# Kernel optimization log

Measured on AMD Instinct MI355X. Metric: run time of the kernel, lower is better.

The kernel has to match this reference:

```python
import jax, jax.numpy as jnp
from jax import lax
import numpy as np

SEQ_LEN = 96; PRED_LEN = 96; SIGNAL_LEN = 16; NUM_NODES = 256
EMBED = 128; HIDDEN = 64; K_NN = 8; S_SCALE = 2.0; CHEB_ORDER = 2
MA_K = 3; BATCH = 16
C_FREQ = SIGNAL_LEN // 2 + 1          # 9 rfft bins
M_NODES = NUM_NODES * C_FREQ          # nodes per sample graph


def _sin_posemb(pos, dim):
    half = dim // 2
    freqs = 1.0 / (10000.0 ** (np.arange(half) / half))
    ang = pos[:, None] * freqs[None, :]
    return np.concatenate([np.sin(ang), np.cos(ang)], axis=-1).astype(np.float32)


def setup_inputs():
    key = jax.random.key(0)
    ks = jax.random.split(key, 12)
    x = jax.random.normal(ks[0], (BATCH, SEQ_LEN, NUM_NODES), jnp.float32)
    # Chebyshev (order 2) approx of Haar framelet filters cos(xi/2), sin(xi/2) on [0, pi]
    t = np.linspace(-1.0, 1.0, 201); xi = (t + 1.0) * np.pi / 2.0
    ch = np.polynomial.chebyshev
    approx = np.stack([ch.chebfit(t, np.cos(xi / 2.0), CHEB_ORDER),
                       ch.chebfit(t, np.sin(xi / 2.0), CHEB_ORDER)]).astype(np.float32)
    freq_emb = _sin_posemb(np.arange(C_FREQ, dtype=np.float32) * S_SCALE, EMBED)
    sc = (2.0 / EMBED) ** 0.5
    return dict(
        x=x,
        approx=jnp.asarray(approx),                 # [F=2, K=3]
        theta=jnp.ones((2,), jnp.float32),
        fr_Wr=jax.random.normal(ks[1], (EMBED, EMBED), jnp.float32) * sc,
        fr_Wi=jax.random.normal(ks[2], (EMBED, EMBED), jnp.float32) * sc,
        eo_Wr=jax.random.normal(ks[3], (1, EMBED), jnp.float32) * sc,
        eo_Wi=jax.random.normal(ks[4], (1, EMBED), jnp.float32) * sc,
        freq_emb=jnp.asarray(freq_emb),             # [C, EMBED]
        n1_w=jnp.ones((NUM_NODES,), jnp.float32), n1_b=jnp.zeros((NUM_NODES,), jnp.float32),
        n2_w=jnp.ones((NUM_NODES,), jnp.float32), n2_b=jnp.zeros((NUM_NODES,), jnp.float32),
        W1_w=jax.random.normal(ks[5], (HIDDEN, SEQ_LEN), jnp.float32) * (1.0 / SEQ_LEN ** 0.5),
        W1_b=jnp.zeros((HIDDEN,), jnp.float32),
        W2_w=jax.random.normal(ks[6], (HIDDEN, HIDDEN), jnp.float32) * (1.0 / HIDDEN ** 0.5),
        W2_b=jnp.zeros((HIDDEN,), jnp.float32),
        Wt_w=jax.random.normal(ks[7], (HIDDEN, SEQ_LEN), jnp.float32) * (1.0 / SEQ_LEN ** 0.5),
        Wt_b=jnp.zeros((HIDDEN,), jnp.float32),
        W3_w=jax.random.normal(ks[8], (PRED_LEN, HIDDEN), jnp.float32) * (1.0 / HIDDEN ** 0.5),
        W3_b=jnp.zeros((PRED_LEN,), jnp.float32),
    )


def _clinear(z, Wr, Wi):
    xr, xi = z.real, z.imag
    return lax.complex(xr @ Wr.T - xi @ Wi.T, xr @ Wi.T + xi @ Wr.T)


def _csilu(z):
    return lax.complex(jax.nn.silu(z.real), jax.nn.silu(z.imag))


def _cheb_prop(h, row, col, ew, coeffs):
    # Chebyshev recurrence with A_norm(h) = scatter_add(row, (ew/s) * h[col])
    w = (ew / S_SCALE)[:, None]
    def A(hh):
        return jnp.zeros_like(hh).at[row].add(w * hh[col])
    Tx0 = h
    out = coeffs[0] * Tx0
    Tx1 = -A(Tx0)
    out = out + coeffs[1] * Tx1
    for ki in range(2, CHEB_ORDER + 1):
        Tx2 = -2.0 * A(Tx1) - Tx0
        out = out + coeffs[ki] * Tx2
        Tx0, Tx1 = Tx1, Tx2
    return out


def _knn_one(feat):
    # feat [M, 2] -> symmetrised degree-normalised KNN edges
    sq = jnp.sum(feat * feat, axis=1)
    d2 = sq[:, None] + sq[None, :] - 2.0 * (feat @ feat.T)
    d2 = jnp.where(jnp.eye(M_NODES, dtype=bool), jnp.inf, d2)
    idx = lax.top_k(-d2, K_NN)[1]                      # smallest distances
    src = jnp.repeat(jnp.arange(M_NODES), K_NN)
    dst = idx.reshape(-1)
    r = jnp.concatenate([src, dst])
    c = jnp.concatenate([dst, src])
    deg = jnp.zeros((M_NODES,), jnp.float32).at[r].add(1.0)
    dinv = (deg + 1e-8) ** -0.5
    return r, c, dinv[r] * dinv[c]


def _moving_avg(x):
    pad = MA_K // 2
    front = jnp.repeat(x[:, :1, :], pad, axis=1)
    back = jnp.repeat(x[:, -1:, :], MA_K - 1 - pad, axis=1)
    xp = jnp.concatenate([front, x, back], axis=1)     # (B, T+k-1, N)
    cs = jnp.cumsum(xp, axis=1)
    cs = jnp.concatenate([jnp.zeros_like(cs[:, :1, :]), cs], axis=1)
    return (cs[:, MA_K:, :] - cs[:, :-MA_K, :]) / MA_K  # (B, T, N)


def _inorm(h, w, b):
    mu = jnp.mean(h, axis=-1, keepdims=True)
    var = jnp.mean((h - mu) ** 2, axis=-1, keepdims=True)
    return (h - mu) / jnp.sqrt(var + 1e-5) * w[None, :, None] + b[None, :, None]


def _forward(x, approx, theta, fr_Wr, fr_Wi, eo_Wr, eo_Wi, freq_emb,
             n1_w, n1_b, n2_w, n2_b, W1_w, W1_b, W2_w, W2_b, Wt_w, Wt_b, W3_w, W3_b):
    B, T, N = x.shape
    trend = _moving_avg(x)
    seasonal = x - trend
    S = jnp.fft.rfft(seasonal, n=SIGNAL_LEN, axis=1, norm='ortho')   # (B, C, N) c64
    S_perm = jnp.transpose(S, (0, 2, 1))                             # (B, N, C)
    node_feat = S_perm[..., None] * freq_emb                         # (B, N, C, E) c64
    batch_x = node_feat.reshape(B * M_NODES, EMBED)
    sg = S_perm.reshape(B, M_NODES)
    feat = lax.stop_gradient(jnp.stack([sg.real, sg.imag], axis=-1))  # (B, M, 2)
    rs, cs_, ews = jax.vmap(_knn_one)(feat)
    off = (jnp.arange(B) * M_NODES)[:, None]
    row = (rs + off).reshape(-1)
    col = (cs_ + off).reshape(-1)
    ew = ews.reshape(-1)
    # framelet layer: sum of F filtered Chebyshev propagations
    acc = jnp.zeros_like(batch_x)
    for i in range(approx.shape[0]):
        acc = acc + theta[i] * _cheb_prop(batch_x, row, col, ew, approx[i])
    h = _csilu(_clinear(acc, fr_Wr, fr_Wi))
    S_out = _clinear(h, eo_Wr, eo_Wi).reshape(B, N, C_FREQ)
    H = jnp.fft.irfft(jnp.transpose(S_out, (0, 2, 1)), n=SEQ_LEN, axis=1, norm='ortho')
    H = jnp.transpose(H, (0, 2, 1))                                  # (B, N, T)
    H = jax.nn.silu(_inorm(H, n1_w, n1_b))
    H = H @ W1_w.T + W1_b
    H = jax.nn.silu(_inorm(H, n2_w, n2_b))
    H = H @ W2_w.T + W2_b
    trend_emb = jnp.transpose(trend, (0, 2, 1)) @ Wt_w.T + Wt_b
    return (H + trend_emb) @ W3_w.T + W3_b                           # (B, N, pred_len)


def reference(x, approx, theta, fr_Wr, fr_Wi, eo_Wr, eo_Wi, freq_emb,
              n1_w, n1_b, n2_w, n2_b, W1_w, W1_b, W2_w, W2_b, Wt_w, Wt_b, W3_w, W3_b):
    return _forward(x, approx, theta, fr_Wr, fr_Wi, eo_Wr, eo_Wi, freq_emb,
                    n1_w, n1_b, n2_w, n2_b, W1_w, W1_b, W2_w, W2_b, Wt_w, Wt_b, W3_w, W3_b)
```

## Files before the change

kernel.cpp:

```cpp
#include <hip/hip_runtime.h>
#include <math.h>
#include <float.h>

#define BATCH 16
#define SEQ 96
#define NNODE 256
#define CFREQ 9
#define MNODE (NNODE * CFREQ)
#define BM (BATCH * MNODE)
#define KNN 8
#define EMBED 128
#define HIDDEN 64
#define TN (SEQ * NNODE)
#define KCAP 64
#define NBLK (BM / 256)
#define HROWS 8
#define PN 64

__constant__ float COS16[16] = {
    1.0f, 0.9238795325112867f, 0.7071067811865476f, 0.3826834323650898f,
    0.0f, -0.3826834323650898f, -0.7071067811865476f, -0.9238795325112867f,
    -1.0f, -0.9238795325112867f, -0.7071067811865476f, -0.3826834323650898f,
    0.0f, 0.3826834323650898f, 0.7071067811865476f, 0.9238795325112867f};
__constant__ float SIN16[16] = {
    0.0f, 0.3826834323650898f, 0.7071067811865476f, 0.9238795325112867f,
    1.0f, 0.9238795325112867f, 0.7071067811865476f, 0.3826834323650898f,
    0.0f, -0.3826834323650898f, -0.7071067811865476f, -0.9238795325112867f,
    -1.0f, -0.9238795325112867f, -0.7071067811865476f, -0.3826834323650898f};

static __device__ __forceinline__ float silu_f(float x) {
    return x / (1.0f + expf(-x));
}

static __device__ __forceinline__ float rank_h(float2 fj, float xi2, float yi2) {
    float sqj = __fmaf_rn(fj.y, fj.y, __fmul_rn(fj.x, fj.x));
    return __fmaf_rn(xi2, fj.x, __fmaf_rn(yi2, fj.y, sqj));
}

__global__ void __launch_bounds__(256) prep_kernel(const float* __restrict__ x,
                                                   float* __restrict__ trend,
                                                   float* __restrict__ S) {
    __shared__ float xs[96][PN];
    __shared__ float ss[16][PN];
    int b = blockIdx.y;
    int n0 = blockIdx.x * PN;
    int tid = threadIdx.x;
    const float* xb = x + b * TN;
    for (int i = tid; i < 96 * PN; i += 256) {
        int t = i >> 6, n = i & 63;
        xs[t][n] = xb[t * NNODE + n0 + n];
    }
    __syncthreads();
    float* tb = trend + b * TN;
    for (int i = tid; i < 96 * PN; i += 256) {
        int t = i >> 6, n = i & 63;
        int tm = t > 0 ? t - 1 : 0;
        int tp = t < SEQ - 1 ? t + 1 : SEQ - 1;
        float v = (xs[tm][n] + xs[t][n] + xs[tp][n]) * (1.0f / 3.0f);
        tb[t * NNODE + n0 + n] = v;
        if (t < 16) ss[t][n] = xs[t][n] - v;
    }
    __syncthreads();
    for (int o = tid; o < PN * CFREQ; o += 256) {
        int n = o / 9, c = o - n * 9;
        float re = 0.0f, im = 0.0f;
        #pragma unroll
        for (int t = 0; t < 16; ++t) {
            float s = ss[t][n];
            int k = (c * t) & 15;
            re += s * COS16[k];
            im -= s * SIN16[k];
        }
        int m = (n0 + n) * CFREQ + c;
        S[(b * MNODE + m) * 2 + 0] = re * 0.25f;
        S[(b * MNODE + m) * 2 + 1] = im * 0.25f;
    }
}

__global__ void __launch_bounds__(256, 8) knn_kernel(const float* __restrict__ S,
                                                     int* __restrict__ idx, int* __restrict__ cnt) {
    __shared__ float2 f[MNODE];
    __shared__ unsigned long long kbuf[4][KCAP];
    int b = blockIdx.y;
    int tid = threadIdx.x;
    for (int t = tid; t < MNODE; t += 256) {
        f[t] = make_float2(S[(b * MNODE + t) * 2 + 0], S[(b * MNODE + t) * 2 + 1]);
    }
    __syncthreads();
    int wave = tid >> 6, lane = tid & 63;
    int i = blockIdx.x * 4 + wave;
    float2 fi = f[i];
    float xi2 = __fmul_rn(-2.0f, fi.x), yi2 = __fmul_rn(-2.0f, fi.y);
    int lane_i = __builtin_amdgcn_readfirstlane(i & 63);
    int k_i    = __builtin_amdgcn_readfirstlane(i >> 6);

    float h[36];
    float mymin = FLT_MAX;
    #pragma unroll
    for (int k = 0; k < 36; ++k) {
        int j = lane + (k << 6);
        float hh = rank_h(f[j], xi2, yi2);
        if (k == k_i && lane == lane_i) hh = FLT_MAX;
        h[k] = hh;
        mymin = fminf(mymin, hh);
    }
    float g = mymin;
    g = fminf(g, __shfl_xor(g, 1, 64));
    g = fminf(g, __shfl_xor(g, 2, 64));
    g = fminf(g, __shfl_xor(g, 4, 64));
    float T = g;
    T = fmaxf(T, __shfl_xor(T, 8, 64));
    T = fmaxf(T, __shfl_xor(T, 16, 64));
    T = fmaxf(T, __shfl_xor(T, 32, 64));
    unsigned long long* mybuf = kbuf[wave];
    const unsigned long long lmask = (1ull << lane) - 1ull;
    int total = 0;
    #pragma unroll
    for (int k = 0; k < 36; ++k) {
        bool pred = h[k] <= T;
        unsigned long long mask = __ballot(pred);
        if (pred) {
            int pos = total + (int)__popcll(mask & lmask);
            if (pos < KCAP) {
                unsigned int bits = __float_as_uint(h[k]);
                if (bits == 0x80000000u) bits = 0u;
                unsigned int s = bits ^ (unsigned int)(((int)bits >> 31) | 0x80000000);
                mybuf[pos] = ((unsigned long long)s << 32) | (unsigned int)(lane + (k << 6));
            }
        }
        total += (int)__popcll(mask);
    }

    if (total >= KNN && total <= KCAP) {
        int padded = (total + 7) & ~7;
        if (lane < padded - total) mybuf[total + lane] = ~0ull;
        for (int p = lane; p < total; p += 64) {
            unsigned long long mykey = mybuf[p];
            int rank = 0;
            for (int q = 0; q < padded; q += 8) {
                const ulonglong2* bp = (const ulonglong2*)&mybuf[q];
                ulonglong2 a = bp[0], b2 = bp[1], c2 = bp[2], d2 = bp[3];
                rank += (int)(a.x  < mykey) + (int)(a.y  < mykey)
                      + (int)(b2.x < mykey) + (int)(b2.y < mykey)
                      + (int)(c2.x < mykey) + (int)(c2.y < mykey)
                      + (int)(d2.x < mykey) + (int)(d2.y < mykey);
            }
            if (rank < KNN) {
                int j = (int)(unsigned int)(mykey & 0xFFFFFFFFull);
                idx[(b * MNODE + i) * KNN + rank] = j;
                atomicAdd(&cnt[b * MNODE + j], 1);
            }
        }
    } else {
        const unsigned long long SENT = ~0ull;
        unsigned long long k0 = SENT, k1 = SENT, k2 = SENT, k3 = SENT,
                           k4 = SENT, k5 = SENT, k6 = SENT, k7 = SENT;
        #pragma unroll
        for (int k = 0; k < 36; ++k) {
            unsigned int bits = __float_as_uint(h[k]);
            if (bits == 0x80000000u) bits = 0u;
            unsigned int s = bits ^ (unsigned int)(((int)bits >> 31) | 0x80000000);
            unsigned long long key = ((unsigned long long)s << 32) | (unsigned int)(lane + (k << 6));
            if (key < k7) {
                k7 = key;
                if (k7 < k6) { unsigned long long t = k6; k6 = k7; k7 = t; }
                if (k6 < k5) { unsigned long long t = k5; k5 = k6; k6 = t; }
                if (k5 < k4) { unsigned long long t = k4; k4 = k5; k5 = t; }
                if (k4 < k3) { unsigned long long t = k3; k3 = k4; k4 = t; }
                if (k3 < k2) { unsigned long long t = k2; k2 = k3; k3 = t; }
                if (k2 < k1) { unsigned long long t = k1; k1 = k2; k2 = t; }
                if (k1 < k0) { unsigned long long t = k0; k0 = k1; k1 = t; }
            }
        }
        unsigned long long mywin = 0;
        #pragma unroll
        for (int r = 0; r < KNN; ++r) {
            unsigned long long hh = k0;
            #pragma unroll
            for (int off = 32; off > 0; off >>= 1) {
                unsigned long long o = __shfl_xor(hh, off, 64);
                if (o < hh) hh = o;
            }
            if (lane == r) mywin = hh;
            if (k0 == hh) {
                k0 = k1; k1 = k2; k2 = k3; k3 = k4; k4 = k5; k5 = k6; k6 = k7; k7 = SENT;
            }
        }
        if (lane < KNN) {
            int j = (int)(unsigned int)(mywin & 0xFFFFFFFFull);
            idx[(b * MNODE + i) * KNN + lane] = j;
            atomicAdd(&cnt[b * MNODE + j], 1);
        }
    }
}

__global__ void __launch_bounds__(256) dinv_scanblk_kernel(
    const int* __restrict__ cnt, const float* __restrict__ S,
    float* __restrict__ dinv, float* __restrict__ PS, int* __restrict__ bsum) {
    __shared__ int wsum[4];
    int tid = threadIdx.x;
    int gid = blockIdx.x * 256 + tid;
    int c = cnt[gid];
    float deg = (float)(KNN + c);
    float dv = 1.0f / sqrtf(deg + 1e-8f);
    dinv[gid] = dv;
    PS[gid * 2 + 0] = dv * S[gid * 2 + 0];
    PS[gid * 2 + 1] = dv * S[gid * 2 + 1];
    int s = c;
    #pragma unroll
    for (int off = 32; off > 0; off >>= 1) s += __shfl_down(s, off, 64);
    if ((tid & 63) == 0) wsum[tid >> 6] = s;
    __syncthreads();
    if (tid == 0) bsum[blockIdx.x] = wsum[0] + wsum[1] + wsum[2] + wsum[3];
}

__global__ void __launch_bounds__(256) scan_apply_kernel(const int* __restrict__ cnt,
                                                         const int* __restrict__ bsum,
                                                         int* __restrict__ offs) {
    __shared__ int wsum[4];
    __shared__ int sbase[4];
    int tid = threadIdx.x;
    int lane = tid & 63, wv = tid >> 6;
    int bb = 0;
    if (tid < NBLK && tid < (int)blockIdx.x) bb = bsum[tid];
    #pragma unroll
    for (int off = 32; off > 0; off >>= 1) bb += __shfl_down(bb, off, 64);
    if (lane == 0) sbase[wv] = bb;
    int gid = blockIdx.x * 256 + tid;
    int v = cnt[gid];
    int x = v;
    #pragma unroll
    for (int off = 1; off < 64; off <<= 1) {
        int y = __shfl_up(x, off, 64);
        if (lane >= off) x += y;
    }
    if (lane == 63) wsum[wv] = x;
    __syncthreads();
    int base = sbase[0] + sbase[1] + sbase[2] + sbase[3];
    for (int w = 0; w < wv; ++w) base += wsum[w];
    offs[gid] = base + x - v;
}

__global__ void fill_kernel(const int* __restrict__ idx, const int* __restrict__ offs,
                            int* __restrict__ fptr, int* __restrict__ rev) {
    int gid = blockIdx.x * blockDim.x + threadIdx.x;
    if (gid >= BM * KNN) return;
    int b = gid / (MNODE * KNN);
    int rem = gid - b * (MNODE * KNN);
    int i = rem / KNN;
    int gj = b * MNODE + idx[gid];
    int pos = atomicAdd(&fptr[gj], 1);
    rev[offs[gj] + pos] = b * MNODE + i;
}

__global__ void __launch_bounds__(256) gather1_kernel(
    const int* __restrict__ idx, const int* __restrict__ offs, const int* __restrict__ cnt,
    const int* __restrict__ rev, const float* __restrict__ dinv, const float* __restrict__ PS,
    float* __restrict__ zA) {
    int gid = blockIdx.x * blockDim.x + threadIdx.x;
    if (gid >= BM * CFREQ) return;
    int gi = gid / CFREQ;
    int c = gid - gi * CFREQ;
    int b = gi / MNODE;
    float ax = 0.0f, ay = 0.0f;
    #pragma unroll
    for (int k = 0; k < KNN; ++k) {
        int gj = b * MNODE + idx[gi * KNN + k];
        bool m = (gj % CFREQ) == c;
        float2 p = ((const float2*)PS)[gj];
        ax += m ? p.x : 0.0f;
        ay += m ? p.y : 0.0f;
    }
    int o = offs[gi], e = o + cnt[gi];
    for (int p_ = o; p_ < e; ++p_) {
        int gk = rev[p_];
        bool m = (gk % CFREQ) == c;
        float2 p = ((const float2*)PS)[gk];
        ax += m ? p.x : 0.0f;
        ay += m ? p.y : 0.0f;
    }
    float s = dinv[gi] * 0.5f;
    zA[gid * 2 + 0] = s * ax;
    zA[gid * 2 + 1] = s * ay;
}

__global__ void __launch_bounds__(256) gather2_kernel(
    const int* __restrict__ idx, const int* __restrict__ offs, const int* __restrict__ cnt,
    const int* __restrict__ rev, const float* __restrict__ dinv, const float* __restrict__ zA,
    float* __restrict__ zB) {
    int gid = blockIdx.x * blockDim.x + threadIdx.x;
    if (gid >= BM * CFREQ) return;
    int gi = gid / CFREQ;
    int c = gid - gi * CFREQ;
    int b = gi / MNODE;
    float ax = 0.0f, ay = 0.0f;
    float di = dinv[gi] * 0.5f;
    #pragma unroll
    for (int k = 0; k < KNN; ++k) {
        int gj = b * MNODE + idx[gi * KNN + k];
        float w = di * dinv[gj];
        float2 v = ((const float2*)zA)[gj * CFREQ + c];
        ax += w * v.x;
        ay += w * v.y;
    }
    int o = offs[gi], e = o + cnt[gi];
    for (int p = o; p < e; ++p) {
        int gk = rev[p];
        float w = di * dinv[gk];
        float2 v = ((const float2*)zA)[gk * CFREQ + c];
        ax += w * v.x;
        ay += w * v.y;
    }
    zB[gid * 2 + 0] = ax;
    zB[gid * 2 + 1] = ay;
}

__global__ void fe_kernel(const float* __restrict__ femb, const float* __restrict__ Wr,
                          const float* __restrict__ Wi, float* __restrict__ FE) {
    int gid = blockIdx.x * blockDim.x + threadIdx.x;
    if (gid >= CFREQ * EMBED) return;
    int c = gid / EMBED;
    int e = gid - c * EMBED;
    float ar = 0.0f, ai = 0.0f;
    for (int k = 0; k < EMBED; ++k) {
        float f = femb[c * EMBED + k];
        ar += f * Wr[e * EMBED + k];
        ai += f * Wi[e * EMBED + k];
    }
    FE[gid * 2 + 0] = ar;
    FE[gid * 2 + 1] = ai;
}

__global__ void __launch_bounds__(256) rowproj_kernel(
    const float* __restrict__ S, const float* __restrict__ zA, const float* __restrict__ zB,
    const float* __restrict__ FE, const float* __restrict__ eoWr, const float* __restrict__ eoWi,
    const float* __restrict__ theta, const float* __restrict__ approx,
    float* __restrict__ Sout) {
    int wave = threadIdx.x >> 6;
    int lane = threadIdx.x & 63;
    int r = blockIdx.x * 4 + wave;
    if (r >= BM) return;
    float a0 = theta[0] * approx[0] + theta[1] * approx[3];
    float a1 = theta[0] * approx[1] + theta[1] * approx[4];
    float a2 = theta[0] * approx[2] + theta[1] * approx[5];
    float ca = a0 - a2, cb = -a1, cc = 2.0f * a2;
    int cr = r % CFREQ;
    float sr = S[r * 2 + 0], si = S[r * 2 + 1];
    int e1 = lane + 64;
    float ur0 = 0.0f, ui0 = 0.0f, ur1 = 0.0f, ui1 = 0.0f;
    #pragma unroll
    for (int c = 0; c < CFREQ; ++c) {
        float zr = cb * zA[(r * CFREQ + c) * 2 + 0] + cc * zB[(r * CFREQ + c) * 2 + 0];
        float zi = cb * zA[(r * CFREQ + c) * 2 + 1] + cc * zB[(r * CFREQ + c) * 2 + 1];
        if (c == cr) { zr += ca * sr; zi += ca * si; }
        float fr0 = FE[(c * EMBED + lane) * 2 + 0], fi0 = FE[(c * EMBED + lane) * 2 + 1];
        float fr1 = FE[(c * EMBED + e1) * 2 + 0],  fi1 = FE[(c * EMBED + e1) * 2 + 1];
        ur0 += zr * fr0 - zi * fi0;  ui0 += zr * fi0 + zi * fr0;
        ur1 += zr * fr1 - zi * fi1;  ui1 += zr * fi1 + zi * fr1;
    }
    float hr0 = silu_f(ur0), hi0 = silu_f(ui0);
    float hr1 = silu_f(ur1), hi1 = silu_f(ui1);
    float wr0 = eoWr[lane], wi0 = eoWi[lane], wr1 = eoWr[e1], wi1 = eoWi[e1];
    float p = hr0 * wr0 - hi0 * wi0 + hr1 * wr1 - hi1 * wi1;
    float q = hr0 * wi0 + hi0 * wr0 + hr1 * wi1 + hi1 * wr1;
    #pragma unroll
    for (int off = 32; off > 0; off >>= 1) {
        p += __shfl_down(p, off, 64);
        q += __shfl_down(q, off, 64);
    }
    if (lane == 0) {
        Sout[r * 2 + 0] = p;
        Sout[r * 2 + 1] = q;
    }
}

__global__ void __launch_bounds__(512) head_kernel(
    const float* __restrict__ Sout, const float* __restrict__ trend,
    const float* __restrict__ n1w, const float* __restrict__ n1b,
    const float* __restrict__ n2w, const float* __restrict__ n2b,
    const float* __restrict__ W1w, const float* __restrict__ W1b,
    const float* __restrict__ W2w, const float* __restrict__ W2b,
    const float* __restrict__ Wtw, const float* __restrict__ Wtb,
    const float* __restrict__ W3w, const float* __restrict__ W3b,
    float* __restrict__ out) {
    __shared__ float tabc[96], tabs[96];
    __shared__ float srow[HROWS][18];
    __shared__ float tbuf[HROWS][96];
    __shared__ float hraw[HROWS][96];
    __shared__ float sH[HROWS][96];
    __shared__ float h2[HROWS][64];
    __shared__ float s3[HROWS][64];
    __shared__ float red[HROWS][2];
    __shared__ float wbuf[6240];
    int tid = threadIdx.x;
    int wave = tid >> 6, lane = tid & 63;
    int bn0 = blockIdx.x * HROWS;
    if (tid < 96) {
        double a = 6.283185307179586476925286766559 * (double)tid / 96.0;
        tabc[tid] = (float)cos(a);
        tabs[tid] = (float)sin(a);
    }
    for (int i = tid; i < HROWS * 96; i += 512) {
        int g = i / 96, t = i - g * 96;
        int bn = bn0 + g;
        tbuf[g][t] = trend[(bn >> 8) * TN + t * NNODE + (bn & 255)];
    }
    if (tid < HROWS * 18) {
        int g = tid / 18, k = tid - g * 18;
        srow[g][k] = Sout[(bn0 + g) * 18 + k];
    }
    __syncthreads();
    for (int i = tid; i < HROWS * 96; i += 512) {
        int g = i / 96, t = i - g * 96;
        float acc = srow[g][0];
        #pragma unroll
        for (int c = 1; c < CFREQ; ++c) {
            int k = (c * t) % 96;
            acc += 2.0f * (srow[g][2 * c] * tabc[k] - srow[g][2 * c + 1] * tabs[k]);
        }
        hraw[g][t] = acc * 0.10206207261596575f;
    }
    __syncthreads();
    {
        float v = hraw[wave][lane] + ((lane < 32) ? hraw[wave][64 + lane] : 0.0f);
        #pragma unroll
        for (int off = 32; off > 0; off >>= 1) v += __shfl_down(v, off, 64);
        if (lane == 0) red[wave][0] = v * (1.0f / 96.0f);
    }
    __syncthreads();
    {
        float mu = red[wave][0];
        float d0 = hraw[wave][lane] - mu;
        float v = d0 * d0;
        if (lane < 32) { float d1 = hraw[wave][64 + lane] - mu; v += d1 * d1; }
        #pragma unroll
        for (int off = 32; off > 0; off >>= 1) v += __shfl_down(v, off, 64);
        if (lane == 0) red[wave][1] = v * (1.0f / 96.0f);
    }
    __syncthreads();
    for (int i = tid; i < HROWS * 96; i += 512) {
        int g = i / 96, t = i - g * 96;
        int n = (bn0 + g) & 255;
        float xn = (hraw[g][t] - red[g][0]) / sqrtf(red[g][1] + 1e-5f) * n1w[n] + n1b[n];
        sH[g][t] = silu_f(xn);
    }
    for (int i = tid; i < HIDDEN * 96; i += 512) {
        int rr = i / 96;
        wbuf[rr * 97 + (i - rr * 96)] = W1w[i];
    }
    __syncthreads();
    float v1;
    {
        float acc = W1b[lane];
        #pragma unroll 8
        for (int t = 0; t < 96; ++t) acc += sH[wave][t] * wbuf[lane * 97 + t];
        v1 = acc;
    }
    {
        float s = v1;
        #pragma unroll
        for (int off = 32; off > 0; off >>= 1) s += __shfl_down(s, off, 64);
        s = __shfl(s, 0, 64);
        float mu2 = s * (1.0f / 64.0f);
        float d = v1 - mu2;
        float vs = d * d;
        #pragma unroll
        for (int off = 32; off > 0; off >>= 1) vs += __shfl_down(vs, off, 64);
        vs = __shfl(vs, 0, 64);
        float var2 = vs * (1.0f / 64.0f);
        int n = (bn0 + wave) & 255;
        float xn = (v1 - mu2) / sqrtf(var2 + 1e-5f) * n2w[n] + n2b[n];
        h2[wave][lane] = silu_f(xn);
    }
    __syncthreads();
    for (int i = tid; i < HIDDEN * HIDDEN; i += 512) {
        wbuf[(i >> 6) * 65 + (i & 63)] = W2w[i];
    }
    __syncthreads();
    float v3;
    {
        float acc = W2b[lane];
        #pragma unroll 8
        for (int h = 0; h < 64; ++h) acc += h2[wave][h] * wbuf[lane * 65 + h];
        v3 = acc;
    }
    __syncthreads();
    for (int i = tid; i < HIDDEN * 96; i += 512) {
        int rr = i / 96;
        wbuf[rr * 97 + (i - rr * 96)] = Wtw[i];
    }
    __syncthreads();
    {
        float acc = Wtb[lane];
        #pragma unroll 8
        for (int t = 0; t < 96; ++t) acc += tbuf[wave][t] * wbuf[lane * 97 + t];
        s3[wave][lane] = v3 + acc;
    }
    __syncthreads();
    for (int i = tid; i < 96 * HIDDEN; i += 512) {
        wbuf[(i >> 6) * 65 + (i & 63)] = W3w[i];
    }
    __syncthreads();
    for (int i = tid; i < HROWS * 96; i += 512) {
        int g = i / 96, t = i - g * 96;
        float acc = W3b[t];
        #pragma unroll 8
        for (int h = 0; h < 64; ++h) acc += s3[g][h] * wbuf[t * 65 + h];
        out[(bn0 + g) * 96 + t] = acc;
    }
}

extern "C" void kernel_launch(void* const* d_in, const int* in_sizes, int n_in,
                              void* d_out, int out_size, void* d_ws, size_t ws_size,
                              hipStream_t stream) {
    const float* x     = (const float*)d_in[0];
    const float* approx= (const float*)d_in[1];
    const float* theta = (const float*)d_in[2];
    const float* frWr  = (const float*)d_in[3];
    const float* frWi  = (const float*)d_in[4];
    const float* eoWr  = (const float*)d_in[5];
    const float* eoWi  = (const float*)d_in[6];
    const float* femb  = (const float*)d_in[7];
    const float* n1w   = (const float*)d_in[8];
    const float* n1b   = (const float*)d_in[9];
    const float* n2w   = (const float*)d_in[10];
    const float* n2b   = (const float*)d_in[11];
    const float* W1w   = (const float*)d_in[12];
    const float* W1b   = (const float*)d_in[13];
    const float* W2w   = (const float*)d_in[14];
    const float* W2b   = (const float*)d_in[15];
    const float* Wtw   = (const float*)d_in[16];
    const float* Wtb   = (const float*)d_in[17];
    const float* W3w   = (const float*)d_in[18];
    const float* W3b   = (const float*)d_in[19];
    float* out = (float*)d_out;

    char* ws = (char*)d_ws;
    size_t off = 0;
    auto alloc = [&](size_t bytes) -> void* {
        void* p = ws + off;
        off = (off + bytes + 255) & ~(size_t)255;
        return p;
    };
    float* trend = (float*)alloc((size_t)BATCH * TN * 4);
    float* S     = (float*)alloc((size_t)BM * 2 * 4);
    int*   idx   = (int*)  alloc((size_t)BM * KNN * 4);
    float* dinv  = (float*)alloc((size_t)BM * 4);
    float* PS    = (float*)alloc((size_t)BM * 2 * 4);
    float* FE    = (float*)alloc((size_t)CFREQ * EMBED * 2 * 4);
    float* Sout  = (float*)alloc((size_t)BM * 2 * 4);
    int*   offs  = (int*)  alloc((size_t)BM * 4);
    int*   rev   = (int*)  alloc((size_t)BM * KNN * 4);
    float* zA    = (float*)alloc((size_t)BM * CFREQ * 2 * 4);
    float* zB    = (float*)alloc((size_t)BM * CFREQ * 2 * 4);
    int*   bsum  = (int*)  alloc((size_t)NBLK * 4);
    char*  zbase = ws + off;
    int*   cnt   = (int*)  alloc((size_t)BM * 4);
    int*   fptr  = (int*)  alloc((size_t)BM * 4);
    size_t zbytes = (size_t)(ws + off - zbase);

    hipMemsetAsync(zbase, 0, zbytes, stream);

    prep_kernel<<<dim3(NNODE / PN, BATCH), 256, 0, stream>>>(x, trend, S);
    knn_kernel<<<dim3(MNODE / 4, BATCH), 256, 0, stream>>>(S, idx, cnt);
    dinv_scanblk_kernel<<<NBLK, 256, 0, stream>>>(cnt, S, dinv, PS, bsum);
    scan_apply_kernel<<<NBLK, 256, 0, stream>>>(cnt, bsum, offs);
    fill_kernel<<<(BM * KNN + 255) / 256, 256, 0, stream>>>(idx, offs, fptr, rev);
    gather1_kernel<<<(BM * CFREQ + 255) / 256, 256, 0, stream>>>(idx, offs, cnt, rev, dinv, PS, zA);
    gather2_kernel<<<(BM * CFREQ + 255) / 256, 256, 0, stream>>>(idx, offs, cnt, rev, dinv, zA, zB);
    fe_kernel<<<(CFREQ * EMBED + 255) / 256, 256, 0, stream>>>(femb, frWr, frWi, FE);
    rowproj_kernel<<<BM / 4, 256, 0, stream>>>(S, zA, zB, FE, eoWr, eoWi, theta, approx, Sout);
    head_kernel<<<BATCH * NNODE / HROWS, 512, 0, stream>>>(Sout, trend, n1w, n1b, n2w, n2b,
                                                           W1w, W1b, W2w, W2b, Wtw, Wtb, W3w, W3b, out);
}
```

Before: 260.9 us.

## Fuse prep/FE kernels, drop memset and trend buffer, pre-scale gather inputs

The prep kernel now computes the DFT per node-frequency straight from x, zeroes cnt and also computes the FE projection, which removes the trend buffer, the memset and the separate fe_kernel launch. The head kernel recomputes the moving-average trend from x in shared memory. scan_apply writes offsets and counts together as an int2 and seeds fptr with the offsets, so fill no longer has to read offs. gather1 also writes a dinv-prescaled copy so gather2 skips the per-neighbor dinv loads, at the cost of an extra BM*9 complex buffer write.

```diff
diff --git a/kernel.cpp b/kernel.cpp
--- a/kernel.cpp
+++ b/kernel.cpp
@@ -15,7 +15,7 @@
 #define KCAP 64
 #define NBLK (BM / 256)
 #define HROWS 8
-#define PN 64
+#define FEW (CFREQ * EMBED)
 
 __constant__ float COS16[16] = {
     1.0f, 0.9238795325112867f, 0.7071067811865476f, 0.3826834323650898f,
@@ -37,43 +37,47 @@
     return __fmaf_rn(xi2, fj.x, __fmaf_rn(yi2, fj.y, sqj));
 }
 
-__global__ void __launch_bounds__(256) prep_kernel(const float* __restrict__ x,
-                                                   float* __restrict__ trend,
-                                                   float* __restrict__ S) {
-    __shared__ float xs[96][PN];
-    __shared__ float ss[16][PN];
-    int b = blockIdx.y;
-    int n0 = blockIdx.x * PN;
-    int tid = threadIdx.x;
-    const float* xb = x + b * TN;
-    for (int i = tid; i < 96 * PN; i += 256) {
-        int t = i >> 6, n = i & 63;
-        xs[t][n] = xb[t * NNODE + n0 + n];
-    }
-    __syncthreads();
-    float* tb = trend + b * TN;
-    for (int i = tid; i < 96 * PN; i += 256) {
-        int t = i >> 6, n = i & 63;
-        int tm = t > 0 ? t - 1 : 0;
-        int tp = t < SEQ - 1 ? t + 1 : SEQ - 1;
-        float v = (xs[tm][n] + xs[t][n] + xs[tp][n]) * (1.0f / 3.0f);
-        tb[t * NNODE + n0 + n] = v;
-        if (t < 16) ss[t][n] = xs[t][n] - v;
-    }
-    __syncthreads();
-    for (int o = tid; o < PN * CFREQ; o += 256) {
-        int n = o / 9, c = o - n * 9;
+__global__ void __launch_bounds__(256) prep_kernel(
+    const float* __restrict__ x, float* __restrict__ S, int* __restrict__ cnt,
+    const float* __restrict__ femb, const float* __restrict__ Wr,
+    const float* __restrict__ Wi, float* __restrict__ FE) {
+    int gid = blockIdx.x * 256 + threadIdx.x;
+    if (gid < BM) {
+        cnt[gid] = 0;
+        int b = gid / MNODE;
+        int m = gid - b * MNODE;
+        int n = m / CFREQ;
+        int c = m - n * CFREQ;
+        const float* xb = x + b * TN + n;
+        float xv[17];
+        #pragma unroll
+        for (int t = 0; t < 17; ++t) xv[t] = xb[t * NNODE];
         float re = 0.0f, im = 0.0f;
         #pragma unroll
         for (int t = 0; t < 16; ++t) {
-            float s = ss[t][n];
+            int tm = t > 0 ? t - 1 : 0;
+            float tr = (xv[tm] + xv[t] + xv[t + 1]) * (1.0f / 3.0f);
+            float s = xv[t] - tr;
             int k = (c * t) & 15;
             re += s * COS16[k];
             im -= s * SIN16[k];
         }
-        int m = (n0 + n) * CFREQ + c;
-        S[(b * MNODE + m) * 2 + 0] = re * 0.25f;
-        S[(b * MNODE + m) * 2 + 1] = im * 0.25f;
+        S[gid * 2 + 0] = re * 0.25f;
+        S[gid * 2 + 1] = im * 0.25f;
+    } else {
+        int f = gid - BM;
+        if (f < FEW) {
+            int c = f / EMBED;
+            int e = f - c * EMBED;
+            float ar = 0.0f, ai = 0.0f;
+            for (int k = 0; k < EMBED; ++k) {
+                float fv = femb[c * EMBED + k];
+                ar += fv * Wr[e * EMBED + k];
+                ai += fv * Wi[e * EMBED + k];
+            }
+            FE[f * 2 + 0] = ar;
+            FE[f * 2 + 1] = ai;
+        }
     }
 }
 
@@ -216,7 +220,8 @@
 
 __global__ void __launch_bounds__(256) scan_apply_kernel(const int* __restrict__ cnt,
                                                          const int* __restrict__ bsum,
-                                                         int* __restrict__ offs) {
+                                                         int2* __restrict__ oc,
+                                                         int* __restrict__ fptr) {
     __shared__ int wsum[4];
     __shared__ int sbase[4];
     int tid = threadIdx.x;
@@ -238,10 +243,12 @@
     __syncthreads();
     int base = sbase[0] + sbase[1] + sbase[2] + sbase[3];
     for (int w = 0; w < wv; ++w) base += wsum[w];
-    offs[gid] = base + x - v;
-}
-
-__global__ void fill_kernel(const int* __restrict__ idx, const int* __restrict__ offs,
+    int o = base + x - v;
+    oc[gid] = make_int2(o, v);
+    fptr[gid] = o;
+}
+
+__global__ void fill_kernel(const int* __restrict__ idx,
                             int* __restrict__ fptr, int* __restrict__ rev) {
     int gid = blockIdx.x * blockDim.x + threadIdx.x;
     if (gid >= BM * KNN) return;
@@ -250,13 +257,13 @@
     int i = rem / KNN;
     int gj = b * MNODE + idx[gid];
     int pos = atomicAdd(&fptr[gj], 1);
-    rev[offs[gj] + pos] = b * MNODE + i;
+    rev[pos] = b * MNODE + i;
 }
 
 __global__ void __launch_bounds__(256) gather1_kernel(
-    const int* __restrict__ idx, const int* __restrict__ offs, const int* __restrict__ cnt,
+    const int* __restrict__ idx, const int2* __restrict__ oc,
     const int* __restrict__ rev, const float* __restrict__ dinv, const float* __restrict__ PS,
-    float* __restrict__ zA) {
+    float* __restrict__ zA, float* __restrict__ zAw) {
     int gid = blockIdx.x * blockDim.x + threadIdx.x;
     if (gid >= BM * CFREQ) return;
     int gi = gid / CFREQ;
@@ -271,7 +278,8 @@
         ax += m ? p.x : 0.0f;
         ay += m ? p.y : 0.0f;
     }
-    int o = offs[gi], e = o + cnt[gi];
+    int2 ocv = oc[gi];
+    int o = ocv.x, e = o + ocv.y;
     for (int p_ = o; p_ < e; ++p_) {
         int gk = rev[p_];
         bool m = (gk % CFREQ) == c;
@@ -279,14 +287,18 @@
         ax += m ? p.x : 0.0f;
         ay += m ? p.y : 0.0f;
     }
-    float s = dinv[gi] * 0.5f;
-    zA[gid * 2 + 0] = s * ax;
-    zA[gid * 2 + 1] = s * ay;
+    float dv = dinv[gi];
+    float s = dv * 0.5f;
+    float zx = s * ax, zy = s * ay;
+    zA[gid * 2 + 0] = zx;
+    zA[gid * 2 + 1] = zy;
+    zAw[gid * 2 + 0] = dv * zx;
+    zAw[gid * 2 + 1] = dv * zy;
 }
 
 __global__ void __launch_bounds__(256) gather2_kernel(
-    const int* __restrict__ idx, const int* __restrict__ offs, const int* __restrict__ cnt,
-    const int* __restrict__ rev, const float* __restrict__ dinv, const float* __restrict__ zA,
+    const int* __restrict__ idx, const int2* __restrict__ oc,
+    const int* __restrict__ rev, const float* __restrict__ dinv, const float* __restrict__ zAw,
     float* __restrict__ zB) {
     int gid = blockIdx.x * blockDim.x + threadIdx.x;
     if (gid >= BM * CFREQ) return;
@@ -294,41 +306,24 @@
     int c = gid - gi * CFREQ;
     int b = gi / MNODE;
     float ax = 0.0f, ay = 0.0f;
-    float di = dinv[gi] * 0.5f;
     #pragma unroll
     for (int k = 0; k < KNN; ++k) {
         int gj = b * MNODE + idx[gi * KNN + k];
-        float w = di * dinv[gj];
-        float2 v = ((const float2*)zA)[gj * CFREQ + c];
-        ax += w * v.x;
-        ay += w * v.y;
-    }
-    int o = offs[gi], e = o + cnt[gi];
+        float2 v = ((const float2*)zAw)[gj * CFREQ + c];
+        ax += v.x;
+        ay += v.y;
+    }
+    int2 ocv = oc[gi];
+    int o = ocv.x, e = o + ocv.y;
     for (int p = o; p < e; ++p) {
         int gk = rev[p];
-        float w = di * dinv[gk];
-        float2 v = ((const float2*)zA)[gk * CFREQ + c];
-        ax += w * v.x;
-        ay += w * v.y;
-    }
-    zB[gid * 2 + 0] = ax;
-    zB[gid * 2 + 1] = ay;
-}
-
-__global__ void fe_kernel(const float* __restrict__ femb, const float* __restrict__ Wr,
-                          const float* __restrict__ Wi, float* __restrict__ FE) {
-    int gid = blockIdx.x * blockDim.x + threadIdx.x;
-    if (gid >= CFREQ * EMBED) return;
-    int c = gid / EMBED;
-    int e = gid - c * EMBED;
-    float ar = 0.0f, ai = 0.0f;
-    for (int k = 0; k < EMBED; ++k) {
-        float f = femb[c * EMBED + k];
-        ar += f * Wr[e * EMBED + k];
-        ai += f * Wi[e * EMBED + k];
-    }
-    FE[gid * 2 + 0] = ar;
-    FE[gid * 2 + 1] = ai;
+        float2 v = ((const float2*)zAw)[gk * CFREQ + c];
+        ax += v.x;
+        ay += v.y;
+    }
+    float s = dinv[gi] * 0.5f;
+    zB[gid * 2 + 0] = s * ax;
+    zB[gid * 2 + 1] = s * ay;
 }
 
 __global__ void __launch_bounds__(256) rowproj_kernel(
@@ -375,7 +370,7 @@
 }
 
 __global__ void __launch_bounds__(512) head_kernel(
-    const float* __restrict__ Sout, const float* __restrict__ trend,
+    const float* __restrict__ Sout, const float* __restrict__ x,
     const float* __restrict__ n1w, const float* __restrict__ n1b,
     const float* __restrict__ n2w, const float* __restrict__ n2b,
     const float* __restrict__ W1w, const float* __restrict__ W1b,
@@ -403,11 +398,18 @@
     for (int i = tid; i < HROWS * 96; i += 512) {
         int g = i / 96, t = i - g * 96;
         int bn = bn0 + g;
-        tbuf[g][t] = trend[(bn >> 8) * TN + t * NNODE + (bn & 255)];
+        hraw[g][t] = x[(bn >> 8) * TN + t * NNODE + (bn & 255)];
     }
     if (tid < HROWS * 18) {
         int g = tid / 18, k = tid - g * 18;
         srow[g][k] = Sout[(bn0 + g) * 18 + k];
+    }
+    __syncthreads();
+    for (int i = tid; i < HROWS * 96; i += 512) {
+        int g = i / 96, t = i - g * 96;
+        int tm = t > 0 ? t - 1 : 0;
+        int tp = t < SEQ - 1 ? t + 1 : SEQ - 1;
+        tbuf[g][t] = (hraw[g][tm] + hraw[g][t] + hraw[g][tp]) * (1.0f / 3.0f);
     }
     __syncthreads();
     for (int i = tid; i < HROWS * 96; i += 512) {
@@ -542,34 +544,29 @@
         off = (off + bytes + 255) & ~(size_t)255;
         return p;
     };
-    float* trend = (float*)alloc((size_t)BATCH * TN * 4);
     float* S     = (float*)alloc((size_t)BM * 2 * 4);
     int*   idx   = (int*)  alloc((size_t)BM * KNN * 4);
     float* dinv  = (float*)alloc((size_t)BM * 4);
     float* PS    = (float*)alloc((size_t)BM * 2 * 4);
-    float* FE    = (float*)alloc((size_t)CFREQ * EMBED * 2 * 4);
+    float* FE    = (float*)alloc((size_t)FEW * 2 * 4);
     float* Sout  = (float*)alloc((size_t)BM * 2 * 4);
-    int*   offs  = (int*)  alloc((size_t)BM * 4);
+    int2*  oc    = (int2*) alloc((size_t)BM * 8);
     int*   rev   = (int*)  alloc((size_t)BM * KNN * 4);
     float* zA    = (float*)alloc((size_t)BM * CFREQ * 2 * 4);
+    float* zAw   = (float*)alloc((size_t)BM * CFREQ * 2 * 4);
     float* zB    = (float*)alloc((size_t)BM * CFREQ * 2 * 4);
     int*   bsum  = (int*)  alloc((size_t)NBLK * 4);
-    char*  zbase = ws + off;
     int*   cnt   = (int*)  alloc((size_t)BM * 4);
     int*   fptr  = (int*)  alloc((size_t)BM * 4);
-    size_t zbytes = (size_t)(ws + off - zbase);
-
-    hipMemsetAsync(zbase, 0, zbytes, stream);
-
-    prep_kernel<<<dim3(NNODE / PN, BATCH), 256, 0, stream>>>(x, trend, S);
+
+    prep_kernel<<<(BM + FEW + 255) / 256, 256, 0, stream>>>(x, S, cnt, femb, frWr, frWi, FE);
     knn_kernel<<<dim3(MNODE / 4, BATCH), 256, 0, stream>>>(S, idx, cnt);
     dinv_scanblk_kernel<<<NBLK, 256, 0, stream>>>(cnt, S, dinv, PS, bsum);
-    scan_apply_kernel<<<NBLK, 256, 0, stream>>>(cnt, bsum, offs);
-    fill_kernel<<<(BM * KNN + 255) / 256, 256, 0, stream>>>(idx, offs, fptr, rev);
-    gather1_kernel<<<(BM * CFREQ + 255) / 256, 256, 0, stream>>>(idx, offs, cnt, rev, dinv, PS, zA);
-    gather2_kernel<<<(BM * CFREQ + 255) / 256, 256, 0, stream>>>(idx, offs, cnt, rev, dinv, zA, zB);
-    fe_kernel<<<(CFREQ * EMBED + 255) / 256, 256, 0, stream>>>(femb, frWr, frWi, FE);
+    scan_apply_kernel<<<NBLK, 256, 0, stream>>>(cnt, bsum, oc, fptr);
+    fill_kernel<<<(BM * KNN + 255) / 256, 256, 0, stream>>>(idx, fptr, rev);
+    gather1_kernel<<<(BM * CFREQ + 255) / 256, 256, 0, stream>>>(idx, oc, rev, dinv, PS, zA, zAw);
+    gather2_kernel<<<(BM * CFREQ + 255) / 256, 256, 0, stream>>>(idx, oc, rev, dinv, zAw, zB);
     rowproj_kernel<<<BM / 4, 256, 0, stream>>>(S, zA, zB, FE, eoWr, eoWi, theta, approx, Sout);
-    head_kernel<<<BATCH * NNODE / HROWS, 512, 0, stream>>>(Sout, trend, n1w, n1b, n2w, n2b,
+    head_kernel<<<BATCH * NNODE / HROWS, 512, 0, stream>>>(Sout, x, n1w, n1b, n2w, n2b,
                                                            W1w, W1b, W2w, W2b, Wtw, Wtb, W3w, W3b, out);
 }
```

After: 248.2 us. 4.9% less time.
